# Optimization experiments

Measured on AMD Instinct MI355X. Metric: run time of the kernel, lower is better.

Reference implementation:

```python
import jax, jax.numpy as jnp
import numpy as np

B, N, L, E = 8, 2000, 128, 2048  # batch, nodes, local_size+1, ff_hidden_dim
PENALTY = 10.0


def setup_inputs() -> dict:
    key = jax.random.key(0)
    ks = jax.random.split(key, 8)
    dist = jax.random.uniform(ks[0], (B, N, N), jnp.float32) + 1e-3  # positive distances
    theta = jax.random.normal(ks[1], (B, N, N), jnp.float32)
    ins_feature0 = jax.random.normal(ks[2], (B, N, 1), jnp.float32)
    ins_feature1 = jax.random.normal(ks[3], (B, N, 1), jnp.float32)
    d_in = 2 * L + 2
    W1 = jax.random.normal(ks[4], (d_in, E), jnp.float32) * 0.02
    b1 = jnp.zeros((E,), jnp.float32)
    W2 = jax.random.normal(ks[5], (E, L), jnp.float32) * 0.02
    b2 = jnp.zeros((L,), jnp.float32)
    return {"theta": theta, "dist": dist, "ins_feature0": ins_feature0,
            "ins_feature1": ins_feature1, "W1": W1, "b1": b1, "W2": W2, "b2": b2}


def reference(theta, dist, ins_feature0, ins_feature1, W1, b1, W2, b2):
    k = W2.shape[1]  # local_size (L)
    # smallest-k along last dim, sorted ascending (torch.topk largest=False)
    neg_vals, idx = jax.lax.top_k(-dist, k)          # [B,N,L]
    sorted_dist = -neg_vals
    sorted_dist = sorted_dist / jnp.max(sorted_dist, axis=-1, keepdims=True)
    sorted_theta = jnp.take_along_axis(theta, idx, axis=-1)  # [B,N,L]
    x_in = jnp.concatenate([sorted_dist, sorted_theta, ins_feature0, ins_feature1], axis=-1)  # [B,N,2L+2]
    edge_emb = x_in @ W1 + b1                        # [B,N,E] (no nonlinearity, as in source)
    out = edge_emb @ W2 + b2 - sorted_dist           # [B,N,L]
    b_, n_, _ = dist.shape
    bi = jnp.arange(b_)[:, None, None]
    ni = jnp.arange(n_)[None, :, None]
    out_mat = jnp.full(dist.shape, PENALTY, dist.dtype).at[bi, ni, idx].set(out)
    return out_mat
```

## Files before the change

kernel.cpp:

```cpp
#include <hip/hip_runtime.h>
#include <hip/hip_bf16.h>

#define BN 8
#define NN 2000
#define LL 128
#define EE 2048
#define DIN 258
#define KPAD 264
#define NROWS (BN*NN)
#define PENALTY_V 10.0f
#define NBINS 512
#define CANDCAP 256
#define SPLITK 16
#define ECHUNK (EE/SPLITK)
#define RPB 4

__global__ __launch_bounds__(256) void kA1(const float* __restrict__ W1,
                                           const float* __restrict__ b1,
                                           const float* __restrict__ W2,
                                           float* __restrict__ part) {
    __shared__ float As2[8][64];
    const int t = threadIdx.x;
    const int j = t & 127;
    const int half = t >> 7;
    const int rg = blockIdx.x >> 4;
    const int ks = blockIdx.x & 15;
    const int k0 = rg * 8;
    const int ebase = ks * ECHUNK;
    float acc[4] = {0.f, 0.f, 0.f, 0.f};
    for (int ec = ebase; ec < ebase + ECHUNK; ec += 64) {
        #pragma unroll
        for (int q = 0; q < 2; ++q) {
            int linear = q * 256 + t;
            int r8 = linear >> 6;
            int e  = linear & 63;
            int k  = k0 + r8;
            float v;
            if (k < DIN)       v = W1[k * EE + ec + e];
            else if (k == DIN) v = b1[ec + e];
            else               v = 0.0f;
            As2[r8][e] = v;
        }
        __syncthreads();
        #pragma unroll 8
        for (int e = 0; e < 64; ++e) {
            float w = W2[(ec + e) * LL + j];
            #pragma unroll
            for (int rr = 0; rr < 4; ++rr)
                acc[rr] += As2[half * 4 + rr][e] * w;
        }
        __syncthreads();
    }
    #pragma unroll
    for (int rr = 0; rr < 4; ++rr) {
        int k = k0 + half * 4 + rr;
        part[(size_t)ks * (KPAD * LL) + k * LL + j] = acc[rr];
    }
}

__global__ __launch_bounds__(256) void kA2(const float* __restrict__ part,
                                           const float* __restrict__ b2,
                                           float* __restrict__ Wc,
                                           float* __restrict__ bc) {
    const int i = blockIdx.x * 256 + threadIdx.x;
    float s = 0.f;
    #pragma unroll
    for (int q = 0; q < SPLITK; ++q) s += part[(size_t)q * (KPAD * LL) + i];
    const int k = i >> 7;
    const int j = i & 127;
    if (k == DIN)      { bc[j] = s + b2[j]; Wc[i] = 0.f; }
    else if (k > DIN)  { Wc[i] = 0.f; }
    else               { Wc[i] = s; }
}

__global__ __launch_bounds__(256) void kB(const float* __restrict__ dist,
                                          const float* __restrict__ theta,
                                          const float* __restrict__ f0,
                                          const float* __restrict__ f1,
                                          float* __restrict__ xin,
                                          int*   __restrict__ gidx) {
    __shared__ __align__(16) unsigned int hist_all[RPB][NBINS];
    __shared__ __align__(16) unsigned long long cand_all[RPB][CANDCAP];
    __shared__ __align__(16) float obuf_all[RPB][2 * LL];
    __shared__ __align__(16) int   oidx_all[RPB][LL];
    __shared__ float sdm[RPB];

    const int t = threadIdx.x;
    const int lane = t & 63;
    const int w = t >> 6;
    const int row = blockIdx.x * RPB + w;

    unsigned int* hist = hist_all[w];
    unsigned long long* cand = cand_all[w];
    float* obuf = obuf_all[w];
    int* oidx = oidx_all[w];

    {
        uint4 z4 = {0u, 0u, 0u, 0u};
        #pragma unroll
        for (int q = 0; q < NBINS / 256; ++q)
            *(uint4*)&hist[(lane + q * 64) * 4] = z4;
        unsigned long long f1v = ~0ULL;
        #pragma unroll
        for (int q = 0; q < CANDCAP / 64; ++q)
            cand[lane + q * 64] = f1v;
    }

    unsigned int v[32];
    const int nv = (lane < 52) ? 32 : 28;
    {
        const uint4* drow4 = (const uint4*)(dist + (size_t)row * NN);
        #pragma unroll
        for (int q = 0; q < 8; ++q) {
            int qi = q * 64 + lane;
            if (qi < NN / 4) {
                uint4 a = drow4[qi];
                v[4 * q]     = a.x;
                v[4 * q + 1] = a.y;
                v[4 * q + 2] = a.z;
                v[4 * q + 3] = a.w;
            }
        }
    }

    unsigned int lmax = 0u;
    #pragma unroll
    for (int k = 0; k < 32; ++k) if (k < nv) lmax = max(lmax, v[k]);
    #pragma unroll
    for (int d = 1; d < 64; d <<= 1) lmax = max(lmax, (unsigned int)__shfl_xor((int)lmax, d));
    const float scale = (float)(NBINS - 1) / __uint_as_float(lmax);

    #pragma unroll
    for (int k = 0; k < 32; ++k) {
        if (k < nv) {
            float f = __uint_as_float(v[k]);
            int b = (int)(f * scale);
            b = b > NBINS - 1 ? NBINS - 1 : b;
            atomicAdd(&hist[b], 1u);
        }
    }

    {
        uint4* h4 = (uint4*)&hist[lane * 8];
        uint4 a0 = h4[0], a1 = h4[1];
        unsigned int c[8] = {a0.x, a0.y, a0.z, a0.w, a1.x, a1.y, a1.z, a1.w};
        unsigned int loc[8], run = 0;
        #pragma unroll
        for (int k = 0; k < 8; ++k) { loc[k] = run; run += c[k]; }
        unsigned int inc = run;
        #pragma unroll
        for (int d = 1; d < 64; d <<= 1) {
            unsigned int o = (unsigned int)__shfl_up((int)inc, d);
            if (lane >= d) inc += o;
        }
        const unsigned int excl = inc - run;
        uint4 s0 = {excl + loc[0], excl + loc[1], excl + loc[2], excl + loc[3]};
        uint4 s1 = {excl + loc[4], excl + loc[5], excl + loc[6], excl + loc[7]};
        h4[0] = s0; h4[1] = s1;
    }

    #pragma unroll
    for (int k = 0; k < 32; ++k) {
        if (k < nv) {
            unsigned int bits = v[k];
            float f = __uint_as_float(bits);
            int b = (int)(f * scale);
            b = b > NBINS - 1 ? NBINS - 1 : b;
            unsigned int old = atomicAdd(&hist[b], 0x10000u);
            unsigned int start = old & 0xFFFFu;
            if (start < (unsigned int)LL) {
                unsigned int slot = start + (old >> 16);
                unsigned int idx = (unsigned int)((k >> 2) * 256 + lane * 4 + (k & 3));
                if (slot < (unsigned int)CANDCAP)
                    cand[slot] = ((unsigned long long)bits << 32) | idx;
            }
        }
    }

    #pragma unroll
    for (int s = 0; s < CANDCAP / 64; ++s) {
        unsigned long long key = cand[lane + s * 64];
        if (key != ~0ULL) {
            unsigned int bits = (unsigned int)(key >> 32);
            unsigned int idx  = (unsigned int)key;
            float th = theta[(size_t)row * NN + idx];
            float f = __uint_as_float(bits);
            int b = (int)(f * scale);
            b = b > NBINS - 1 ? NBINS - 1 : b;
            unsigned int word = hist[b];
            unsigned int start = word & 0xFFFFu;
            unsigned int end = start + (word >> 16);
            if (end > (unsigned int)CANDCAP) end = (unsigned int)CANDCAP;
            unsigned int r = start;
            for (unsigned int j = start; j < end; ++j) r += (cand[j] < key);
            if (r < (unsigned int)LL) {
                obuf[r] = f;
                obuf[LL + r] = th;
                oidx[r] = (int)idx;
                if (r == LL - 1) sdm[w] = f;
            }
        }
    }

    {
        const float rdm = 1.0f / sdm[w];
        float* xrow = xin + (size_t)row * KPAD;
        float4 o = *(float4*)&obuf[lane * 4];
        if (lane < 32) { o.x *= rdm; o.y *= rdm; o.z *= rdm; o.w *= rdm; }
        *(float4*)&xrow[lane * 4] = o;
        if (lane == 0) {
            xrow[256] = f0[row];
            xrow[257] = f1[row];
            #pragma unroll
            for (int z = DIN; z < KPAD; ++z) xrow[z] = 0.0f;
        }
        int2 g = *(int2*)&oidx[lane * 2];
        *(int2*)&gidx[(size_t)row * LL + lane * 2] = g;
    }
}

__global__ __launch_bounds__(256) void kC(const float* __restrict__ xin,
                                          const float* __restrict__ Wc,
                                          const float* __restrict__ bc,
                                          float* __restrict__ val) {
    __shared__ __align__(16) float As[8][132];
    __shared__ __align__(16) float Bs[8][128];
    const int t = threadIdx.x;
    const int tr = t >> 4, tc = t & 15;
    const int row0 = blockIdx.x * 128;
    float acc[8][8];
    #pragma unroll
    for (int i = 0; i < 8; ++i)
        #pragma unroll
        for (int j = 0; j < 8; ++j) acc[i][j] = 0.f;

    for (int kc = 0; kc < KPAD; kc += 8) {
        #pragma unroll
        for (int q = 0; q < 4; ++q) {
            int linear = q * 256 + t;
            int m = linear >> 3, k = linear & 7;
            As[k][m] = xin[(size_t)(row0 + m) * KPAD + kc + k];
        }
        #pragma unroll
        for (int q = 0; q < 4; ++q) {
            int linear = q * 256 + t;
            int k = linear >> 7, c = linear & 127;
            Bs[k][c] = Wc[(kc + k) * LL + c];
        }
        __syncthreads();
        #pragma unroll
        for (int k = 0; k < 8; ++k) {
            float a[8], b[8];
            *(float4*)&a[0] = *(const float4*)&As[k][tr * 8];
            *(float4*)&a[4] = *(const float4*)&As[k][tr * 8 + 4];
            *(float4*)&b[0] = *(const float4*)&Bs[k][tc * 8];
            *(float4*)&b[4] = *(const float4*)&Bs[k][tc * 8 + 4];
            #pragma unroll
            for (int i = 0; i < 8; ++i)
                #pragma unroll
                for (int j = 0; j < 8; ++j)
                    acc[i][j] += a[i] * b[j];
        }
        __syncthreads();
    }
    #pragma unroll
    for (int i = 0; i < 8; ++i) {
        int r = row0 + tr * 8 + i;
        #pragma unroll
        for (int j = 0; j < 8; ++j) {
            int c = tc * 8 + j;
            val[(size_t)r * LL + c] = acc[i][j] + bc[c] - xin[(size_t)r * KPAD + c];
        }
    }
}

__global__ __launch_bounds__(256) void kD(const int* __restrict__ gidx,
                                          const float* __restrict__ val,
                                          float* __restrict__ out) {
    __shared__ __align__(16) float rowbuf[NN];
    const int t = threadIdx.x;
    const int row = blockIdx.x;
    for (int i = t; i < NN; i += 256) rowbuf[i] = PENALTY_V;
    __syncthreads();
    if (t < 128) rowbuf[gidx[(size_t)row * LL + t]] = val[(size_t)row * LL + t];
    __syncthreads();
    float4* out4 = (float4*)(out + (size_t)row * NN);
    const float4* rb4 = (const float4*)rowbuf;
    for (int q = t; q < NN / 4; q += 256) out4[q] = rb4[q];
}

extern "C" void kernel_launch(void* const* d_in, const int* in_sizes, int n_in,
                              void* d_out, int out_size, void* d_ws, size_t ws_size,
                              hipStream_t stream) {
    const float* theta = (const float*)d_in[0];
    const float* dist  = (const float*)d_in[1];
    const float* f0    = (const float*)d_in[2];
    const float* f1    = (const float*)d_in[3];
    const float* W1    = (const float*)d_in[4];
    const float* b1    = (const float*)d_in[5];
    const float* W2    = (const float*)d_in[6];
    const float* b2    = (const float*)d_in[7];
    float* out = (float*)d_out;

    char* ws = (char*)d_ws;
    float* Wc   = (float*)ws;
    float* bc   = (float*)(ws + 135168);
    float* xin  = (float*)(ws + 135680);
    int*   gidx = (int*)  (ws + 135680 + 16896000);
    float* val  = (float*)(ws + 135680 + 16896000 + 8192000);
    float* part = val;

    kA1<<<33 * SPLITK, 256, 0, stream>>>(W1, b1, W2, part);
    kA2<<<(KPAD * LL) / 256, 256, 0, stream>>>(part, b2, Wc, bc);
    kB<<<NROWS / RPB, 256, 0, stream>>>(dist, theta, f0, f1, xin, gidx);
    kC<<<NROWS / 128, 256, 0, stream>>>(xin, Wc, bc, val);
    kD<<<NROWS, 256, 0, stream>>>(gidx, val, out);
}
```

Measured before the change: 145.3 us.

## Prefilter top-k candidates with threshold search before histogram binning

Before histogramming, each wave iteratively searches for a threshold T that keeps between 128 and 384 candidates, using a ballot-style bitmask count with wave reduction. Only the elements below T go through the histogram and scatter atomics, and the bins now span just [0,T] instead of [0,max], which sharpens bin resolution. The theta gathers are also issued in a batch ahead of the rank loop. The aim is fewer LDS atomics and fewer collisions within a bin, at the cost of extra threshold iterations that each rescan all 32 register values.

```diff
diff --git a/kernel.cpp b/kernel.cpp
--- a/kernel.cpp
+++ b/kernel.cpp
@@ -10,7 +10,7 @@
 #define NROWS (BN*NN)
 #define PENALTY_V 10.0f
 #define NBINS 512
-#define CANDCAP 256
+#define CANDCAP 384
 #define SPLITK 16
 #define ECHUNK (EE/SPLITK)
 #define RPB 4
@@ -96,14 +96,12 @@
     int* oidx = oidx_all[w];
 
     {
+        unsigned long long f1v = ~0ULL;
+        #pragma unroll
+        for (int q = 0; q < CANDCAP / 64; ++q) cand[lane + q * 64] = f1v;
         uint4 z4 = {0u, 0u, 0u, 0u};
-        #pragma unroll
-        for (int q = 0; q < NBINS / 256; ++q)
-            *(uint4*)&hist[(lane + q * 64) * 4] = z4;
-        unsigned long long f1v = ~0ULL;
-        #pragma unroll
-        for (int q = 0; q < CANDCAP / 64; ++q)
-            cand[lane + q * 64] = f1v;
+        *(uint4*)&hist[lane * 8] = z4;
+        *(uint4*)&hist[lane * 8 + 4] = z4;
     }
 
     unsigned int v[32];
@@ -128,13 +126,43 @@
     for (int k = 0; k < 32; ++k) if (k < nv) lmax = max(lmax, v[k]);
     #pragma unroll
     for (int d = 1; d < 64; d <<= 1) lmax = max(lmax, (unsigned int)__shfl_xor((int)lmax, d));
-    const float scale = (float)(NBINS - 1) / __uint_as_float(lmax);
-
-    #pragma unroll
-    for (int k = 0; k < 32; ++k) {
-        if (k < nv) {
+    const float vmaxf = __uint_as_float(lmax);
+
+    float lo = 0.0f, hi = vmaxf;
+    float T = vmaxf * 0.128f;
+    unsigned int qm = 0u;
+    bool ok = false;
+    for (int it = 0; it < 32; ++it) {
+        unsigned int m = 0u;
+        #pragma unroll
+        for (int k = 0; k < 32; ++k)
+            if (k < nv && __uint_as_float(v[k]) <= T) m |= (1u << k);
+        int c = __builtin_popcount(m);
+        #pragma unroll
+        for (int d = 1; d < 64; d <<= 1) c += __shfl_xor(c, d);
+        qm = m;
+        if (c >= LL && c <= CANDCAP) { ok = true; break; }
+        if (c < LL) lo = T; else hi = T;
+        float Ts = T * (256.0f / (float)(c > 16 ? c : 16));
+        T = (Ts > lo && Ts < hi) ? Ts : 0.5f * (lo + hi);
+    }
+    if (!ok) {
+        T = hi;
+        unsigned int m = 0u;
+        #pragma unroll
+        for (int k = 0; k < 32; ++k)
+            if (k < nv && __uint_as_float(v[k]) <= T) m |= (1u << k);
+        qm = m;
+    }
+    const float scale2 = (float)(NBINS - 1) / T;
+
+    {
+        unsigned int m = qm;
+        while (m) {
+            int k = __builtin_ctz(m);
+            m &= m - 1u;
             float f = __uint_as_float(v[k]);
-            int b = (int)(f * scale);
+            int b = (int)(f * scale2);
             b = b > NBINS - 1 ? NBINS - 1 : b;
             atomicAdd(&hist[b], 1u);
         }
@@ -159,45 +187,53 @@
         h4[0] = s0; h4[1] = s1;
     }
 
-    #pragma unroll
-    for (int k = 0; k < 32; ++k) {
-        if (k < nv) {
+    {
+        unsigned int m = qm;
+        while (m) {
+            int k = __builtin_ctz(m);
+            m &= m - 1u;
             unsigned int bits = v[k];
             float f = __uint_as_float(bits);
-            int b = (int)(f * scale);
+            int b = (int)(f * scale2);
             b = b > NBINS - 1 ? NBINS - 1 : b;
             unsigned int old = atomicAdd(&hist[b], 0x10000u);
-            unsigned int start = old & 0xFFFFu;
-            if (start < (unsigned int)LL) {
-                unsigned int slot = start + (old >> 16);
-                unsigned int idx = (unsigned int)((k >> 2) * 256 + lane * 4 + (k & 3));
-                if (slot < (unsigned int)CANDCAP)
-                    cand[slot] = ((unsigned long long)bits << 32) | idx;
-            }
-        }
-    }
-
-    #pragma unroll
-    for (int s = 0; s < CANDCAP / 64; ++s) {
-        unsigned long long key = cand[lane + s * 64];
-        if (key != ~0ULL) {
-            unsigned int bits = (unsigned int)(key >> 32);
-            unsigned int idx  = (unsigned int)key;
-            float th = theta[(size_t)row * NN + idx];
-            float f = __uint_as_float(bits);
-            int b = (int)(f * scale);
-            b = b > NBINS - 1 ? NBINS - 1 : b;
-            unsigned int word = hist[b];
-            unsigned int start = word & 0xFFFFu;
-            unsigned int end = start + (word >> 16);
-            if (end > (unsigned int)CANDCAP) end = (unsigned int)CANDCAP;
-            unsigned int r = start;
-            for (unsigned int j = start; j < end; ++j) r += (cand[j] < key);
-            if (r < (unsigned int)LL) {
-                obuf[r] = f;
-                obuf[LL + r] = th;
-                oidx[r] = (int)idx;
-                if (r == LL - 1) sdm[w] = f;
+            unsigned int slot = (old & 0xFFFFu) + (old >> 16);
+            unsigned int idx = (unsigned int)((k >> 2) * 256 + lane * 4 + (k & 3));
+            if (slot < (unsigned int)CANDCAP)
+                cand[slot] = ((unsigned long long)bits << 32) | idx;
+        }
+    }
+
+    {
+        unsigned long long key_s[CANDCAP / 64];
+        float th_s[CANDCAP / 64];
+        #pragma unroll
+        for (int s = 0; s < CANDCAP / 64; ++s) key_s[s] = cand[lane + s * 64];
+        #pragma unroll
+        for (int s = 0; s < CANDCAP / 64; ++s)
+            if (key_s[s] != ~0ULL)
+                th_s[s] = theta[(size_t)row * NN + (unsigned int)key_s[s]];
+        #pragma unroll
+        for (int s = 0; s < CANDCAP / 64; ++s) {
+            unsigned long long key = key_s[s];
+            if (key != ~0ULL) {
+                unsigned int bits = (unsigned int)(key >> 32);
+                unsigned int idx  = (unsigned int)key;
+                float f = __uint_as_float(bits);
+                int b = (int)(f * scale2);
+                b = b > NBINS - 1 ? NBINS - 1 : b;
+                unsigned int word = hist[b];
+                unsigned int start = word & 0xFFFFu;
+                unsigned int end = start + (word >> 16);
+                if (end > (unsigned int)CANDCAP) end = (unsigned int)CANDCAP;
+                unsigned int r = start;
+                for (unsigned int j = start; j < end; ++j) r += (cand[j] < key);
+                if (r < (unsigned int)LL) {
+                    obuf[r] = f;
+                    obuf[LL + r] = th_s[s];
+                    oidx[r] = (int)idx;
+                    if (r == LL - 1) sdm[w] = f;
+                }
             }
         }
     }
```

Result: slower. 151.4 us (+4.2%).
